# Kernel optimization log

Measured on AMD Instinct MI355X. Metric: run time of the kernel, lower is better.

Reference implementation:

```python
import jax, jax.numpy as jnp
import numpy as np

MATCH_IOU = 0.5
IGNORE_IOU = 0.4
BOX_VARIANCE = jnp.asarray([0.1, 0.1, 0.2, 0.2], dtype=jnp.float32)
BACKGROUND_CLASS = -1.0
IGNORE_CLASS = -2.0

M_ANCHORS = 76725  # RetinaNet P3-P7 on 640x640, 9 anchors/loc
BATCH = 16
N_GT = 100
NUM_CLASSES = 20


def setup_inputs() -> dict:
    key = jax.random.key(0)
    k1, k2, k3, k4, k5 = jax.random.split(key, 5)
    # anchors in xywh (top-left x, y, width, height)
    axy = jax.random.uniform(k1, (M_ANCHORS, 2), minval=0.0, maxval=600.0)
    awh = jax.random.uniform(k2, (M_ANCHORS, 2), minval=16.0, maxval=256.0)
    anchor_boxes = jnp.concatenate([axy, awh], axis=-1).astype(jnp.float32)
    # gt boxes [B, N, 5] = [x, y, w, h, class_id] in xywh
    gxy = jax.random.uniform(k3, (BATCH, N_GT, 2), minval=0.0, maxval=600.0)
    gwh = jax.random.uniform(k4, (BATCH, N_GT, 2), minval=8.0, maxval=200.0)
    gcls = jax.random.randint(k5, (BATCH, N_GT, 1), 0, NUM_CLASSES).astype(jnp.float32)
    gt_boxes = jnp.concatenate([gxy, gwh, gcls], axis=-1)
    return {"anchor_boxes": anchor_boxes, "gt_boxes": gt_boxes}


def _xywh_to_corners(b):
    x, y, w, h = b[..., 0], b[..., 1], b[..., 2], b[..., 3]
    return x, y, x + w, y + h


def _pairwise_iou(anchors, gt):
    # anchors: [M, 4], gt: [B, N, 4] -> iou: [B, M, N]
    ax1, ay1, ax2, ay2 = _xywh_to_corners(anchors)          # [M]
    gx1, gy1, gx2, gy2 = _xywh_to_corners(gt)               # [B, N]
    ax1 = ax1[None, :, None]; ay1 = ay1[None, :, None]
    ax2 = ax2[None, :, None]; ay2 = ay2[None, :, None]
    gx1 = gx1[:, None, :]; gy1 = gy1[:, None, :]
    gx2 = gx2[:, None, :]; gy2 = gy2[:, None, :]
    iw = jnp.maximum(jnp.minimum(ax2, gx2) - jnp.maximum(ax1, gx1), 0.0)
    ih = jnp.maximum(jnp.minimum(ay2, gy2) - jnp.maximum(ay1, gy1), 0.0)
    inter = iw * ih                                          # [B, M, N]
    a_area = (anchors[:, 2] * anchors[:, 3])[None, :, None]
    g_area = (gt[..., 2] * gt[..., 3])[:, None, :]
    union = a_area + g_area - inter
    return jnp.where(union > 0.0, inter / union, 0.0)


def reference(anchor_boxes, gt_boxes):
    # anchor_boxes: [M, 4] xywh; gt_boxes: [B, N, 5] xywh + class
    gt_xywh = gt_boxes[..., :4]
    cls_ids = gt_boxes[..., 4]                               # [B, N]

    iou = _pairwise_iou(anchor_boxes, gt_xywh)               # [B, M, N]
    max_iou = jnp.max(iou, axis=-1)                          # [B, M]
    matched_gt_idx = jnp.argmax(iou, axis=-1)                # [B, M]
    positive_mask = max_iou >= MATCH_IOU
    negative_mask = max_iou < IGNORE_IOU
    ignore_mask = jnp.logical_not(positive_mask | negative_mask)

    # gather matched gt boxes / classes: [B, M, 5]
    matched = jnp.take_along_axis(gt_boxes, matched_gt_idx[..., None], axis=1)
    mx, my, mw, mh = matched[..., 0], matched[..., 1], matched[..., 2], matched[..., 3]
    matched_cls = matched[..., 4]

    # encode xywh -> center deltas, scaled by variance
    acx = anchor_boxes[:, 0] + 0.5 * anchor_boxes[:, 2]
    acy = anchor_boxes[:, 1] + 0.5 * anchor_boxes[:, 3]
    aw = anchor_boxes[:, 2]
    ah = anchor_boxes[:, 3]
    gcx = mx + 0.5 * mw
    gcy = my + 0.5 * mh
    box_target = jnp.stack(
        [
            (gcx - acx[None, :]) / aw[None, :],
            (gcy - acy[None, :]) / ah[None, :],
            jnp.log(mw / aw[None, :]),
            jnp.log(mh / ah[None, :]),
        ],
        axis=-1,
    ) / BOX_VARIANCE                                          # [B, M, 4]

    cls_target = jnp.where(positive_mask, matched_cls, BACKGROUND_CLASS)
    cls_target = jnp.where(ignore_mask, IGNORE_CLASS, cls_target)

    label = jnp.concatenate([box_target, cls_target[..., None]], axis=-1)  # [B, M, 5]
    any_nan = jnp.any(jnp.isnan(label), axis=-1, keepdims=True)
    label = jnp.where(any_nan, IGNORE_CLASS, label)
    return label
```

## Files before the change

### kernel.cpp

```cpp
#include <hip/hip_runtime.h>
#include <math.h>

#define M_ANCHORS 76725
#define BATCH     16
#define N_GT      100
#define MATCH_IOU  0.5f
#define IGNORE_IOU 0.4f

__global__ __launch_bounds__(128) void retina_encode_kernel(
    const float* __restrict__ anchors,
    const float* __restrict__ gt,
    float* __restrict__ out)
{
#pragma clang fp contract(off)
    __shared__ float4 s_box[N_GT];
    __shared__ float  s_ga[N_GT];
    __shared__ float  s_raw[N_GT * 5];

    const int b = blockIdx.y;
    const int t = threadIdx.x;
    const int a = blockIdx.x * 128 + t;

    for (int i = t; i < N_GT * 5; i += 128)
        s_raw[i] = gt[b * (N_GT * 5) + i];
    __syncthreads();
    if (t < N_GT) {
        const float gx = s_raw[t * 5 + 0];
        const float gy = s_raw[t * 5 + 1];
        const float gw = s_raw[t * 5 + 2];
        const float gh = s_raw[t * 5 + 3];
        s_box[t] = make_float4(gx, gy, gx + gw, gy + gh);
        s_ga[t]  = gw * gh;
    }
    __syncthreads();

    if (a >= M_ANCHORS) return;

    const float4 av = *reinterpret_cast<const float4*>(anchors + (size_t)a * 4);
    const float ax1 = av.x, ay1 = av.y, aw = av.z, ah = av.w;
    const float ax2 = ax1 + aw;
    const float ay2 = ay1 + ah;
    const float aarea = aw * ah;

    float bI = 0.0f;
    float bS = 1.0f;
    int   bj = 0;
    bool  flag = false;

    #pragma unroll
    for (int j = 0; j < N_GT; ++j) {
        const float4 g = s_box[j];
        const float iw = fmaxf(fminf(ax2, g.z) - fmaxf(ax1, g.x), 0.0f);
        const float ih = fminf(ay2, g.w) - fmaxf(ay1, g.y);
        const float inter = iw * ih;
        const float S   = aarea + s_ga[j];
        const float pb  = bI * S;
        const float d   = fmaf(inter, bS, -pb);
        const float tol = fmaf(4e-6f, pb, -1e-33f);
        flag = flag | (fabsf(d) <= tol);
        if (d > 0.0f) { bI = inter; bS = S; bj = j; }
    }

    float M;
    int bidx = bj;
    if (!flag) {
        M = bI / (bS - bI);
    } else {
        float best = -1.0f;
        bidx = 0;
        #pragma unroll 1
        for (int j = 0; j < N_GT; ++j) {
            const float4 g = s_box[j];
            const float iw = fmaxf(fminf(ax2, g.z) - fmaxf(ax1, g.x), 0.0f);
            const float ih = fmaxf(fminf(ay2, g.w) - fmaxf(ay1, g.y), 0.0f);
            const float inter = iw * ih;
            const float uni = (aarea + s_ga[j]) - inter;
            const float iou = (uni > 0.0f) ? (inter / uni) : 0.0f;
            if (iou > best) { best = iou; bidx = j; }
        }
        M = best;
    }

    const float mx   = s_raw[bidx * 5 + 0];
    const float my   = s_raw[bidx * 5 + 1];
    const float mw   = s_raw[bidx * 5 + 2];
    const float mh   = s_raw[bidx * 5 + 3];
    const float mcls = s_raw[bidx * 5 + 4];

    const float acx = ax1 + 0.5f * aw;
    const float acy = ay1 + 0.5f * ah;
    const float gcx = mx + 0.5f * mw;
    const float gcy = my + 0.5f * mh;

    float t0 = ((gcx - acx) / aw) * 10.0f;
    float t1 = ((gcy - acy) / ah) * 10.0f;
    float t2 = logf(mw / aw) * 5.0f;
    float t3 = logf(mh / ah) * 5.0f;

    const bool pos = (M >= MATCH_IOU);
    const bool neg = (M < IGNORE_IOU);
    float cls = pos ? mcls : -1.0f;
    if (!pos && !neg) cls = -2.0f;

    if (isnan(t0) || isnan(t1) || isnan(t2) || isnan(t3) || isnan(cls)) {
        t0 = t1 = t2 = t3 = cls = -2.0f;
    }

    float* o = out + ((size_t)b * M_ANCHORS + a) * 5;
    o[0] = t0;
    o[1] = t1;
    o[2] = t2;
    o[3] = t3;
    o[4] = cls;
}

extern "C" void kernel_launch(void* const* d_in, const int* in_sizes, int n_in,
                              void* d_out, int out_size, void* d_ws, size_t ws_size,
                              hipStream_t stream) {
    const float* anchors = (const float*)d_in[0];
    const float* gt      = (const float*)d_in[1];
    float* out           = (float*)d_out;

    const dim3 block(128, 1, 1);
    const dim3 grid((M_ANCHORS + 127) / 128, BATCH, 1);
    retina_encode_kernel<<<grid, block, 0, stream>>>(anchors, gt, out);
}
```

Measured before the change: 77.16 us.

## Broadcast GT boxes via readlane from registers instead of LDS loads

Each lane of a wavefront holds up to two GT boxes in registers, and the main IoU loop broadcasts them with readlane (scalar values) instead of reading shared memory. This replaces LDS traffic in the 100-iteration hot loop with SGPR operands. Threads past the end of the anchor array are clamped so the whole wave stays active for readlane, and they return only after the loop. The block size also grows from 128 to 256 threads. The change costs some extra registers and readlane instructions.

```diff
diff --git a/kernel.cpp b/kernel.cpp
--- a/kernel.cpp
+++ b/kernel.cpp
@@ -4,10 +4,16 @@
 #define M_ANCHORS 76725
 #define BATCH     16
 #define N_GT      100
+#define TPB       256
 #define MATCH_IOU  0.5f
 #define IGNORE_IOU 0.4f
 
-__global__ __launch_bounds__(128) void retina_encode_kernel(
+
+__device__ __forceinline__ float rdl(float v, int l) {
+    return __int_as_float(__builtin_amdgcn_readlane(__float_as_int(v), l));
+}
+
+__global__ __launch_bounds__(TPB) void retina_encode_kernel(
     const float* __restrict__ anchors,
     const float* __restrict__ gt,
     float* __restrict__ out)
@@ -19,9 +25,12 @@
 
     const int b = blockIdx.y;
     const int t = threadIdx.x;
-    const int a = blockIdx.x * 128 + t;
+    const int lane = t & 63;
+    const int a_raw = blockIdx.x * TPB + t;
+    const bool valid = (a_raw < M_ANCHORS);
+    const int a = valid ? a_raw : (M_ANCHORS - 1);
 
-    for (int i = t; i < N_GT * 5; i += 128)
+    for (int i = t; i < N_GT * 5; i += TPB)
         s_raw[i] = gt[b * (N_GT * 5) + i];
     __syncthreads();
     if (t < N_GT) {
@@ -34,7 +43,19 @@
     }
     __syncthreads();
 
-    if (a >= M_ANCHORS) return;
+    const int rA = lane;
+    const int rB = (lane + 64 < N_GT) ? (lane + 64) : 0;
+    float Ax1, Ay1, Ax2, Ay2, Aga, Bx1, By1, Bx2, By2, Bga;
+    {
+        const float gx = s_raw[rA * 5 + 0], gy = s_raw[rA * 5 + 1];
+        const float gw = s_raw[rA * 5 + 2], gh = s_raw[rA * 5 + 3];
+        Ax1 = gx; Ay1 = gy; Ax2 = gx + gw; Ay2 = gy + gh; Aga = gw * gh;
+    }
+    {
+        const float gx = s_raw[rB * 5 + 0], gy = s_raw[rB * 5 + 1];
+        const float gw = s_raw[rB * 5 + 2], gh = s_raw[rB * 5 + 3];
+        Bx1 = gx; By1 = gy; Bx2 = gx + gw; By2 = gy + gh; Bga = gw * gh;
+    }
 
     const float4 av = *reinterpret_cast<const float4*>(anchors + (size_t)a * 4);
     const float ax1 = av.x, ay1 = av.y, aw = av.z, ah = av.w;
@@ -49,17 +70,23 @@
 
     #pragma unroll
     for (int j = 0; j < N_GT; ++j) {
-        const float4 g = s_box[j];
-        const float iw = fmaxf(fminf(ax2, g.z) - fmaxf(ax1, g.x), 0.0f);
-        const float ih = fminf(ay2, g.w) - fmaxf(ay1, g.y);
+        const float gx1 = rdl(j < 64 ? Ax1 : Bx1, j & 63);
+        const float gy1 = rdl(j < 64 ? Ay1 : By1, j & 63);
+        const float gx2 = rdl(j < 64 ? Ax2 : Bx2, j & 63);
+        const float gy2 = rdl(j < 64 ? Ay2 : By2, j & 63);
+        const float ga  = rdl(j < 64 ? Aga : Bga, j & 63);
+        const float iw = fmaxf(fminf(ax2, gx2) - fmaxf(ax1, gx1), 0.0f);
+        const float ih = fminf(ay2, gy2) - fmaxf(ay1, gy1);
         const float inter = iw * ih;
-        const float S   = aarea + s_ga[j];
+        const float S   = aarea + ga;
         const float pb  = bI * S;
         const float d   = fmaf(inter, bS, -pb);
         const float tol = fmaf(4e-6f, pb, -1e-33f);
         flag = flag | (fabsf(d) <= tol);
         if (d > 0.0f) { bI = inter; bS = S; bj = j; }
     }
+
+    if (!valid) return;
 
     float M;
     int bidx = bj;
@@ -106,7 +133,7 @@
         t0 = t1 = t2 = t3 = cls = -2.0f;
     }
 
-    float* o = out + ((size_t)b * M_ANCHORS + a) * 5;
+    float* o = out + ((size_t)b * M_ANCHORS + a_raw) * 5;
     o[0] = t0;
     o[1] = t1;
     o[2] = t2;
@@ -121,7 +148,7 @@
     const float* gt      = (const float*)d_in[1];
     float* out           = (float*)d_out;
 
-    const dim3 block(128, 1, 1);
-    const dim3 grid((M_ANCHORS + 127) / 128, BATCH, 1);
+    const dim3 block(TPB, 1, 1);
+    const dim3 grid((M_ANCHORS + TPB - 1) / TPB, BATCH, 1);
     retina_encode_kernel<<<grid, block, 0, stream>>>(anchors, gt, out);
 }
```

Result: slower. 186.2 us (+141.3%).

## Precompute GT corners in prep kernel and read them as uniform global loads

Applied to the files above, without the earlier changes.

Adds a small prep kernel that converts GT boxes to corner form and areas in a workspace buffer. The main kernel drops its shared-memory staging and both barriers and reads the GT data straight from global memory. Because the index depends only on blockIdx, these reads can become scalar loads through the scalar cache. Block size also goes from 128 to 256 threads. The trade-off is an extra kernel launch and reliance on scalar-cache hits inside the 100-step unrolled loop.

```diff
diff --git a/kernel.cpp b/kernel.cpp
--- a/kernel.cpp
+++ b/kernel.cpp
@@ -4,37 +4,42 @@
 #define M_ANCHORS 76725
 #define BATCH     16
 #define N_GT      100
+#define TPB       256
 #define MATCH_IOU  0.5f
 #define IGNORE_IOU 0.4f
 
-__global__ __launch_bounds__(128) void retina_encode_kernel(
+
+__global__ __launch_bounds__(128) void retina_prep_kernel(
+    const float* __restrict__ gt,
+    float4* __restrict__ corn,
+    float* __restrict__ garea)
+{
+#pragma clang fp contract(off)
+    const int i = blockIdx.x * 128 + threadIdx.x;
+    if (i < BATCH * N_GT) {
+        const float gx = gt[i * 5 + 0];
+        const float gy = gt[i * 5 + 1];
+        const float gw = gt[i * 5 + 2];
+        const float gh = gt[i * 5 + 3];
+        corn[i]  = make_float4(gx, gy, gx + gw, gy + gh);
+        garea[i] = gw * gh;
+    }
+}
+
+__global__ __launch_bounds__(TPB) void retina_encode_kernel(
     const float* __restrict__ anchors,
     const float* __restrict__ gt,
+    const float4* __restrict__ corn,
+    const float* __restrict__ garea,
     float* __restrict__ out)
 {
 #pragma clang fp contract(off)
-    __shared__ float4 s_box[N_GT];
-    __shared__ float  s_ga[N_GT];
-    __shared__ float  s_raw[N_GT * 5];
+    const int b = blockIdx.y;
+    const int a = blockIdx.x * TPB + threadIdx.x;
+    if (a >= M_ANCHORS) return;
 
-    const int b = blockIdx.y;
-    const int t = threadIdx.x;
-    const int a = blockIdx.x * 128 + t;
-
-    for (int i = t; i < N_GT * 5; i += 128)
-        s_raw[i] = gt[b * (N_GT * 5) + i];
-    __syncthreads();
-    if (t < N_GT) {
-        const float gx = s_raw[t * 5 + 0];
-        const float gy = s_raw[t * 5 + 1];
-        const float gw = s_raw[t * 5 + 2];
-        const float gh = s_raw[t * 5 + 3];
-        s_box[t] = make_float4(gx, gy, gx + gw, gy + gh);
-        s_ga[t]  = gw * gh;
-    }
-    __syncthreads();
-
-    if (a >= M_ANCHORS) return;
+    const float4* __restrict__ cb = corn  + b * N_GT;
+    const float*  __restrict__ gb = garea + b * N_GT;
 
     const float4 av = *reinterpret_cast<const float4*>(anchors + (size_t)a * 4);
     const float ax1 = av.x, ay1 = av.y, aw = av.z, ah = av.w;
@@ -49,11 +54,12 @@
 
     #pragma unroll
     for (int j = 0; j < N_GT; ++j) {
-        const float4 g = s_box[j];
+        const float4 g  = cb[j];
+        const float  ga = gb[j];
         const float iw = fmaxf(fminf(ax2, g.z) - fmaxf(ax1, g.x), 0.0f);
         const float ih = fminf(ay2, g.w) - fmaxf(ay1, g.y);
         const float inter = iw * ih;
-        const float S   = aarea + s_ga[j];
+        const float S   = aarea + ga;
         const float pb  = bI * S;
         const float d   = fmaf(inter, bS, -pb);
         const float tol = fmaf(4e-6f, pb, -1e-33f);
@@ -70,22 +76,23 @@
         bidx = 0;
         #pragma unroll 1
         for (int j = 0; j < N_GT; ++j) {
-            const float4 g = s_box[j];
+            const float4 g = cb[j];
             const float iw = fmaxf(fminf(ax2, g.z) - fmaxf(ax1, g.x), 0.0f);
             const float ih = fmaxf(fminf(ay2, g.w) - fmaxf(ay1, g.y), 0.0f);
             const float inter = iw * ih;
-            const float uni = (aarea + s_ga[j]) - inter;
+            const float uni = (aarea + gb[j]) - inter;
             const float iou = (uni > 0.0f) ? (inter / uni) : 0.0f;
             if (iou > best) { best = iou; bidx = j; }
         }
         M = best;
     }
 
-    const float mx   = s_raw[bidx * 5 + 0];
-    const float my   = s_raw[bidx * 5 + 1];
-    const float mw   = s_raw[bidx * 5 + 2];
-    const float mh   = s_raw[bidx * 5 + 3];
-    const float mcls = s_raw[bidx * 5 + 4];
+    const float* __restrict__ mrow = gt + ((size_t)b * N_GT + bidx) * 5;
+    const float mx   = mrow[0];
+    const float my   = mrow[1];
+    const float mw   = mrow[2];
+    const float mh   = mrow[3];
+    const float mcls = mrow[4];
 
     const float acx = ax1 + 0.5f * aw;
     const float acy = ay1 + 0.5f * ah;
@@ -121,7 +128,13 @@
     const float* gt      = (const float*)d_in[1];
     float* out           = (float*)d_out;
 
-    const dim3 block(128, 1, 1);
-    const dim3 grid((M_ANCHORS + 127) / 128, BATCH, 1);
-    retina_encode_kernel<<<grid, block, 0, stream>>>(anchors, gt, out);
+    float4* corn  = (float4*)d_ws;
+    float*  garea = (float*)((char*)d_ws + BATCH * N_GT * sizeof(float4));
+
+    retina_prep_kernel<<<dim3((BATCH * N_GT + 127) / 128), dim3(128), 0, stream>>>(
+        gt, corn, garea);
+
+    const dim3 block(TPB, 1, 1);
+    const dim3 grid((M_ANCHORS + TPB - 1) / TPB, BATCH, 1);
+    retina_encode_kernel<<<grid, block, 0, stream>>>(anchors, gt, corn, garea, out);
 }
```

Result: slower. 82.89 us (+7.4%).

## Process two anchors per thread and prefetch ground-truth boxes from LDS

Applied to the files above, without the earlier changes.

Each thread now evaluates two anchors against the 100 ground-truth boxes, so every shared-memory box load serves two IoU comparisons. The running best-match updates for the two anchors form two independent dependency chains, which adds instruction-level parallelism. Box corners and areas are read four at a time, with the next group loaded before the current group is computed. The block grows to 256 threads with an occupancy hint in the launch bounds. In exchange, register pressure rises, and the out-of-range second anchor in the last block has to be clamped and masked.

```diff
diff --git a/kernel.cpp b/kernel.cpp
--- a/kernel.cpp
+++ b/kernel.cpp
@@ -4,24 +4,26 @@
 #define M_ANCHORS 76725
 #define BATCH     16
 #define N_GT      100
+#define TPB       256
 #define MATCH_IOU  0.5f
 #define IGNORE_IOU 0.4f
 
-__global__ __launch_bounds__(128) void retina_encode_kernel(
+
+__global__ __launch_bounds__(TPB, 6) void retina_encode_kernel(
     const float* __restrict__ anchors,
     const float* __restrict__ gt,
     float* __restrict__ out)
 {
 #pragma clang fp contract(off)
-    __shared__ float4 s_box[N_GT];
-    __shared__ float  s_ga[N_GT];
+    __shared__ float4 s_corn[N_GT];
+    __shared__ float4 s_area4[N_GT / 4];
     __shared__ float  s_raw[N_GT * 5];
 
     const int b = blockIdx.y;
     const int t = threadIdx.x;
-    const int a = blockIdx.x * 128 + t;
+    const int base = blockIdx.x * (TPB * 2);
 
-    for (int i = t; i < N_GT * 5; i += 128)
+    for (int i = t; i < N_GT * 5; i += TPB)
         s_raw[i] = gt[b * (N_GT * 5) + i];
     __syncthreads();
     if (t < N_GT) {
@@ -29,89 +31,125 @@
         const float gy = s_raw[t * 5 + 1];
         const float gw = s_raw[t * 5 + 2];
         const float gh = s_raw[t * 5 + 3];
-        s_box[t] = make_float4(gx, gy, gx + gw, gy + gh);
-        s_ga[t]  = gw * gh;
+        s_corn[t] = make_float4(gx, gy, gx + gw, gy + gh);
+        ((float*)s_area4)[t] = gw * gh;
     }
     __syncthreads();
 
-    if (a >= M_ANCHORS) return;
+    const int a0 = base + t;
+    const int a1r = base + TPB + t;
+    const bool v1 = (a1r < M_ANCHORS);
+    const int a1 = v1 ? a1r : (M_ANCHORS - 1);
 
-    const float4 av = *reinterpret_cast<const float4*>(anchors + (size_t)a * 4);
-    const float ax1 = av.x, ay1 = av.y, aw = av.z, ah = av.w;
-    const float ax2 = ax1 + aw;
-    const float ay2 = ay1 + ah;
-    const float aarea = aw * ah;
+    const float4 A0 = *reinterpret_cast<const float4*>(anchors + (size_t)a0 * 4);
+    const float4 A1 = *reinterpret_cast<const float4*>(anchors + (size_t)a1 * 4);
+    const float ax1_0 = A0.x, ay1_0 = A0.y, aw_0 = A0.z, ah_0 = A0.w;
+    const float ax2_0 = ax1_0 + aw_0, ay2_0 = ay1_0 + ah_0, aarea_0 = aw_0 * ah_0;
+    const float ax1_1 = A1.x, ay1_1 = A1.y, aw_1 = A1.z, ah_1 = A1.w;
+    const float ax2_1 = ax1_1 + aw_1, ay2_1 = ay1_1 + ah_1, aarea_1 = aw_1 * ah_1;
 
-    float bI = 0.0f;
-    float bS = 1.0f;
-    int   bj = 0;
-    bool  flag = false;
+    float bI0 = 0.0f, bS0 = 1.0f; int bj0 = 0; bool fl0 = false;
+    float bI1 = 0.0f, bS1 = 1.0f; int bj1 = 0; bool fl1 = false;
+
+#define COMP(G, GAV, J, bI, bS, bj, fl, AX1, AY1, AX2, AY2, AAREA)           \
+    {                                                                        \
+        const float iw = fmaxf(fminf(AX2, (G).z) - fmaxf(AX1, (G).x), 0.0f); \
+        const float ih = fminf(AY2, (G).w) - fmaxf(AY1, (G).y);              \
+        const float inter = iw * ih;                                         \
+        const float S   = AAREA + (GAV);                                     \
+        const float pb  = bI * S;                                            \
+        const float d   = fmaf(inter, bS, -pb);                              \
+        const float tol = fmaf(4e-6f, pb, -1e-33f);                          \
+        fl = fl | (fabsf(d) <= tol);                                         \
+        if (d > 0.0f) { bI = inter; bS = S; bj = (J); }                      \
+    }
+
+#define COMP2(G, GAV, J)                                                       \
+    COMP(G, GAV, J, bI0, bS0, bj0, fl0, ax1_0, ay1_0, ax2_0, ay2_0, aarea_0)   \
+    COMP(G, GAV, J, bI1, bS1, bj1, fl1, ax1_1, ay1_1, ax2_1, ay2_1, aarea_1)
+
+    float4 c0 = s_corn[0], c1 = s_corn[1], c2 = s_corn[2], c3 = s_corn[3];
+    float4 ga = s_area4[0];
 
     #pragma unroll
-    for (int j = 0; j < N_GT; ++j) {
-        const float4 g = s_box[j];
-        const float iw = fmaxf(fminf(ax2, g.z) - fmaxf(ax1, g.x), 0.0f);
-        const float ih = fminf(ay2, g.w) - fmaxf(ay1, g.y);
-        const float inter = iw * ih;
-        const float S   = aarea + s_ga[j];
-        const float pb  = bI * S;
-        const float d   = fmaf(inter, bS, -pb);
-        const float tol = fmaf(4e-6f, pb, -1e-33f);
-        flag = flag | (fabsf(d) <= tol);
-        if (d > 0.0f) { bI = inter; bS = S; bj = j; }
+    for (int jb = 0; jb < 25; ++jb) {
+        float4 n0, n1, n2, n3, nga;
+        if (jb < 24) {
+            n0  = s_corn[jb * 4 + 4];
+            n1  = s_corn[jb * 4 + 5];
+            n2  = s_corn[jb * 4 + 6];
+            n3  = s_corn[jb * 4 + 7];
+            nga = s_area4[jb + 1];
+        }
+        const int j0 = jb * 4;
+        COMP2(c0, ga.x, j0 + 0)
+        COMP2(c1, ga.y, j0 + 1)
+        COMP2(c2, ga.z, j0 + 2)
+        COMP2(c3, ga.w, j0 + 3)
+        c0 = n0; c1 = n1; c2 = n2; c3 = n3; ga = nga;
     }
+#undef COMP2
+#undef COMP
 
-    float M;
-    int bidx = bj;
-    if (!flag) {
-        M = bI / (bS - bI);
-    } else {
-        float best = -1.0f;
-        bidx = 0;
-        #pragma unroll 1
-        for (int j = 0; j < N_GT; ++j) {
-            const float4 g = s_box[j];
-            const float iw = fmaxf(fminf(ax2, g.z) - fmaxf(ax1, g.x), 0.0f);
-            const float ih = fmaxf(fminf(ay2, g.w) - fmaxf(ay1, g.y), 0.0f);
-            const float inter = iw * ih;
-            const float uni = (aarea + s_ga[j]) - inter;
-            const float iou = (uni > 0.0f) ? (inter / uni) : 0.0f;
-            if (iou > best) { best = iou; bidx = j; }
+    auto finish = [&](float bI, float bS, int bj, bool fl,
+                      float ax1, float ay1, float aw, float ah,
+                      float ax2, float ay2, float aarea, int a) {
+        float M;
+        int bidx = bj;
+        if (!fl) {
+            M = bI / (bS - bI);
+        } else {
+            float best = -1.0f;
+            bidx = 0;
+            #pragma unroll 1
+            for (int j = 0; j < N_GT; ++j) {
+                const float4 g = s_corn[j];
+                const float iw = fmaxf(fminf(ax2, g.z) - fmaxf(ax1, g.x), 0.0f);
+                const float ih = fmaxf(fminf(ay2, g.w) - fmaxf(ay1, g.y), 0.0f);
+                const float inter = iw * ih;
+                const float uni = (aarea + ((const float*)s_area4)[j]) - inter;
+                const float iou = (uni > 0.0f) ? (inter / uni) : 0.0f;
+                if (iou > best) { best = iou; bidx = j; }
+            }
+            M = best;
         }
-        M = best;
-    }
 
-    const float mx   = s_raw[bidx * 5 + 0];
-    const float my   = s_raw[bidx * 5 + 1];
-    const float mw   = s_raw[bidx * 5 + 2];
-    const float mh   = s_raw[bidx * 5 + 3];
-    const float mcls = s_raw[bidx * 5 + 4];
+        const float mx   = s_raw[bidx * 5 + 0];
+        const float my   = s_raw[bidx * 5 + 1];
+        const float mw   = s_raw[bidx * 5 + 2];
+        const float mh   = s_raw[bidx * 5 + 3];
+        const float mcls = s_raw[bidx * 5 + 4];
 
-    const float acx = ax1 + 0.5f * aw;
-    const float acy = ay1 + 0.5f * ah;
-    const float gcx = mx + 0.5f * mw;
-    const float gcy = my + 0.5f * mh;
+        const float acx = ax1 + 0.5f * aw;
+        const float acy = ay1 + 0.5f * ah;
+        const float gcx = mx + 0.5f * mw;
+        const float gcy = my + 0.5f * mh;
 
-    float t0 = ((gcx - acx) / aw) * 10.0f;
-    float t1 = ((gcy - acy) / ah) * 10.0f;
-    float t2 = logf(mw / aw) * 5.0f;
-    float t3 = logf(mh / ah) * 5.0f;
+        float t0 = ((gcx - acx) / aw) * 10.0f;
+        float t1 = ((gcy - acy) / ah) * 10.0f;
+        float t2 = logf(mw / aw) * 5.0f;
+        float t3 = logf(mh / ah) * 5.0f;
 
-    const bool pos = (M >= MATCH_IOU);
-    const bool neg = (M < IGNORE_IOU);
-    float cls = pos ? mcls : -1.0f;
-    if (!pos && !neg) cls = -2.0f;
+        const bool pos = (M >= MATCH_IOU);
+        const bool neg = (M < IGNORE_IOU);
+        float cls = pos ? mcls : -1.0f;
+        if (!pos && !neg) cls = -2.0f;
 
-    if (isnan(t0) || isnan(t1) || isnan(t2) || isnan(t3) || isnan(cls)) {
-        t0 = t1 = t2 = t3 = cls = -2.0f;
-    }
+        if (isnan(t0) || isnan(t1) || isnan(t2) || isnan(t3) || isnan(cls)) {
+            t0 = t1 = t2 = t3 = cls = -2.0f;
+        }
 
-    float* o = out + ((size_t)b * M_ANCHORS + a) * 5;
-    o[0] = t0;
-    o[1] = t1;
-    o[2] = t2;
-    o[3] = t3;
-    o[4] = cls;
+        float* o = out + ((size_t)b * M_ANCHORS + a) * 5;
+        o[0] = t0;
+        o[1] = t1;
+        o[2] = t2;
+        o[3] = t3;
+        o[4] = cls;
+    };
+
+    finish(bI0, bS0, bj0, fl0, ax1_0, ay1_0, aw_0, ah_0, ax2_0, ay2_0, aarea_0, a0);
+    if (v1)
+        finish(bI1, bS1, bj1, fl1, ax1_1, ay1_1, aw_1, ah_1, ax2_1, ay2_1, aarea_1, a1);
 }
 
 extern "C" void kernel_launch(void* const* d_in, const int* in_sizes, int n_in,
@@ -121,7 +159,7 @@
     const float* gt      = (const float*)d_in[1];
     float* out           = (float*)d_out;
 
-    const dim3 block(128, 1, 1);
-    const dim3 grid((M_ANCHORS + 127) / 128, BATCH, 1);
+    const dim3 block(TPB, 1, 1);
+    const dim3 grid((M_ANCHORS + TPB * 2 - 1) / (TPB * 2), BATCH, 1);
     retina_encode_kernel<<<grid, block, 0, stream>>>(anchors, gt, out);
 }
```

Result: slower. 204.2 us (+164.7%).
